# Kernel optimization log

Measured on AMD Instinct MI355X. Metric: run time of the kernel, lower is better.

The kernel has to match this reference:

```python
import jax, jax.numpy as jnp
import numpy as np

V, E, H, L = 32000, 1024, 1024, 2
B, T = 64, 256


def setup_inputs() -> dict:
    key = jax.random.key(0)
    ks = jax.random.split(key, 6)
    src = jax.random.randint(ks[0], (B, T), 0, V, dtype=jnp.int32)
    s_e = 1.0 / np.sqrt(H)
    emb = jax.random.normal(ks[1], (V, E), dtype=jnp.float32) * 0.02
    # stacked-layer LSTM params; layer 0 input = E == H so shapes are uniform
    W_ih = jax.random.uniform(ks[2], (L, 4 * H, H), dtype=jnp.float32, minval=-s_e, maxval=s_e)
    W_hh = jax.random.uniform(ks[3], (L, 4 * H, H), dtype=jnp.float32, minval=-s_e, maxval=s_e)
    b_ih = jax.random.uniform(ks[4], (L, 4 * H), dtype=jnp.float32, minval=-s_e, maxval=s_e)
    b_hh = jax.random.uniform(ks[5], (L, 4 * H), dtype=jnp.float32, minval=-s_e, maxval=s_e)
    return {"src": src, "emb": emb, "W_ih": W_ih, "W_hh": W_hh, "b_ih": b_ih, "b_hh": b_hh}


def _lstm_stack(embedded, W_ih, W_hh, b_ih, b_hh):
    # embedded: [B, T, E]
    Bsz = embedded.shape[0]
    h0 = jnp.zeros((L, Bsz, H), embedded.dtype)
    c0 = jnp.zeros((L, Bsz, H), embedded.dtype)

    def step(carry, x_t):
        h, c = carry  # each [L, B, H]
        x = x_t       # [B, E]
        new_h, new_c = [], []
        for l in range(L):
            gates = x @ W_ih[l].T + b_ih[l] + h[l] @ W_hh[l].T + b_hh[l]  # [B, 4H]
            i, f, g, o = jnp.split(gates, 4, axis=-1)
            c_t = jax.nn.sigmoid(f) * c[l] + jax.nn.sigmoid(i) * jnp.tanh(g)
            h_t = jax.nn.sigmoid(o) * jnp.tanh(c_t)
            new_h.append(h_t)
            new_c.append(c_t)
            x = h_t  # feed to next layer (dropout p=0)
        return (jnp.stack(new_h), jnp.stack(new_c)), x

    (h_n, c_n), outs = jax.lax.scan(step, (h0, c0), jnp.swapaxes(embedded, 0, 1))
    return jnp.swapaxes(outs, 0, 1), h_n, c_n  # [B,T,H], [L,B,H], [L,B,H]


def reference(src, emb, W_ih, W_hh, b_ih, b_hh):
    embedded = emb[src]  # [B, T, E]
    encoder_outputs, h_n, c_n = _lstm_stack(embedded, W_ih, W_hh, b_ih, b_hh)
    return encoder_outputs, (h_n, c_n)
```

## Files before the change

kernel.cpp:

```cpp
#include <hip/hip_runtime.h>
#include <hip/hip_bf16.h>

typedef __hip_bfloat16 bf16;
typedef __attribute__((ext_vector_type(8))) short s16x8;
typedef __attribute__((ext_vector_type(4))) float f32x4;
typedef __attribute__((ext_vector_type(4))) int   i32x4;

#define BATCH   64
#define SEQ     256
#define HID     1024
#define GATES   4096
#define NWG     256
#define THREADS 256
#define UNITS   8
#define NCOLS   32
#define ROWSTRIDE 2056
#define GSTRIDE 33
#define BH      (BATCH * HID)

#define H0_SLOTS 4
#define H1_SLOTS 2
#define FLAG_ELEMS ((size_t)6 * BH)
#define WS_BYTES  (FLAG_ELEMS * 2 + 256 * 4)

#define OUT_HN  ((size_t)BATCH * SEQ * HID)
#define OUT_CN  (OUT_HN + 2ull * BATCH * HID)

__device__ __forceinline__ short f2bf(float f) {
    unsigned int u = __builtin_bit_cast(unsigned int, f);
    u = (u + 0x7fffu + ((u >> 16) & 1u)) >> 16;
    return (short)u;
}

__device__ __forceinline__ void st8(void* p, float lo, float hi) {
    union { float f[2]; unsigned long long u; } v;
    v.f[0] = lo; v.f[1] = hi;
    __hip_atomic_store((unsigned long long*)p, v.u, __ATOMIC_RELAXED, __HIP_MEMORY_SCOPE_AGENT);
}

#define MM8(B0) \
    _Pragma("unroll") \
    for (int kk = (B0); kk < (B0) + 8; ++kk) { \
        s16x8 b0 = *(const s16x8*)(s0 + kk * 32); \
        s16x8 b1 = *(const s16x8*)(s1 + kk * 32); \
        s16x8 av = __builtin_bit_cast(s16x8, h[kk]); \
        a0 = __builtin_amdgcn_mfma_f32_16x16x32_bf16(av, b0, a0, 0, 0, 0); \
        a1 = __builtin_amdgcn_mfma_f32_16x16x32_bf16(av, b1, a1, 0, 0, 0); \
    }

__device__ __forceinline__ void gemm_bt(const bf16* xrow, const bf16* s0, const bf16* s1,
                                        f32x4& a0, f32x4& a1)
{
    i32x4 h[32];
#define LD(i, OFF) asm volatile("global_load_dwordx4 %0, %1, off offset:" OFF " sc0" \
                                : "=v"(h[i]) : "v"(xrow))
    LD(0, "0");    LD(1, "64");   LD(2, "128");  LD(3, "192");
    LD(4, "256");  LD(5, "320");  LD(6, "384");  LD(7, "448");
    LD(8, "512");  LD(9, "576");  LD(10, "640"); LD(11, "704");
    LD(12, "768"); LD(13, "832"); LD(14, "896"); LD(15, "960");
    LD(16, "1024"); LD(17, "1088"); LD(18, "1152"); LD(19, "1216");
    LD(20, "1280"); LD(21, "1344"); LD(22, "1408"); LD(23, "1472");
    asm volatile("s_waitcnt vmcnt(16)"); __builtin_amdgcn_sched_barrier(0);
    MM8(0)
    LD(24, "1536"); LD(25, "1600"); LD(26, "1664"); LD(27, "1728");
    LD(28, "1792"); LD(29, "1856"); LD(30, "1920"); LD(31, "1984");
    asm volatile("s_waitcnt vmcnt(16)"); __builtin_amdgcn_sched_barrier(0);
    MM8(8)
    asm volatile("s_waitcnt vmcnt(8)");  __builtin_amdgcn_sched_barrier(0);
    MM8(16)
    asm volatile("s_waitcnt vmcnt(0)");  __builtin_amdgcn_sched_barrier(0);
    MM8(24)
#undef LD
}

__device__ __forceinline__ void wait_dual(unsigned int* flags, int tid, int tgtA, int tgtB) {
    const int tgt = (tid < 128) ? tgtA : tgtB;
    if (tgt > 0) {
        unsigned int* p = flags + tid;
        while ((int)__hip_atomic_load(p, __ATOMIC_RELAXED, __HIP_MEMORY_SCOPE_AGENT) < tgt)
            __builtin_amdgcn_s_sleep(1);
    }
    __syncthreads();
    asm volatile("" ::: "memory");
}

__global__ void ws_init(unsigned int* p, int n) {
    for (int i = blockIdx.x * blockDim.x + threadIdx.x; i < n; i += gridDim.x * blockDim.x)
        p[i] = 0u;
}

__global__ void __launch_bounds__(THREADS, 1)
lstm_enc(const int* __restrict__ src, const float* __restrict__ Wemb,
         const float* __restrict__ Wih, const float* __restrict__ Whh,
         const float* __restrict__ bih, const float* __restrict__ bhh,
         float* __restrict__ out, bf16* __restrict__ hbuf)
{
    __shared__ __align__(16) bf16 slab[NCOLS][ROWSTRIDE];
    __shared__ float gates[BATCH][GSTRIDE];
    __shared__ float bias[NCOLS];

    const int wg    = blockIdx.x;
    const int layer = wg >> 7;
    const int wgl   = wg & 127;
    const int j0    = wgl * UNITS;
    const int tid   = threadIdx.x;
    const int lane  = tid & 63;
    const int wave  = tid >> 6;
    const int m     = lane & 15;
    const int kq    = (lane >> 4) * 8;
    const int b_a   = wave * 16 + m;

    for (int r = 0; r < NCOLS; ++r) {
        int g = r >> 3, u = r & 7;
        size_t grow = (size_t)layer * GATES * HID + (size_t)(g * HID + j0 + u) * HID;
        int k = tid * 8;
        const float* s = (k < HID) ? (Wih + grow + k) : (Whh + grow + (k - HID));
        s16x8 v;
#pragma unroll
        for (int j = 0; j < 8; ++j) v[j] = f2bf(s[j]);
        *(s16x8*)&slab[r][k] = v;
    }
    if (tid < NCOLS) {
        int g = tid >> 3, u = tid & 7;
        int off = layer * GATES + g * HID + j0 + u;
        bias[tid] = bih[off] + bhh[off];
    }
    __syncthreads();

    __builtin_amdgcn_fence(__ATOMIC_ACQUIRE, "agent");

    bf16* h0 = hbuf;
    bf16* h1 = hbuf + H0_SLOTS * BH;
    unsigned int* flags = (unsigned int*)(hbuf + FLAG_ELEMS);

    const int bb = tid >> 2;
    const int u0 = (tid & 3) * 2;
    float c_lo = 0.f, c_hi = 0.f;

    int sv = (layer == 0) ? src[b_a * SEQ] : 0;

    for (int t = 0; t < SEQ; ++t) {
        f32x4 acc0 = {0.f, 0.f, 0.f, 0.f};
        f32x4 acc1 = {0.f, 0.f, 0.f, 0.f};

        if (layer == 0) {
            const float* xF = Wemb + (size_t)sv * HID + kq;
            if (t + 1 < SEQ) sv = src[b_a * SEQ + t + 1];
#pragma unroll
            for (int c = 0; c < 4; ++c) {
                f32x4 xv[16];
#pragma unroll
                for (int i = 0; i < 8; ++i) {
                    const float* p = xF + (c * 8 + i) * 32;
                    xv[2 * i]     = *(const f32x4*)p;
                    xv[2 * i + 1] = *(const f32x4*)(p + 4);
                }
#pragma unroll
                for (int i = 0; i < 8; ++i) {
                    const int k = (c * 8 + i) * 32 + kq;
                    s16x8 af;
#pragma unroll
                    for (int j = 0; j < 4; ++j) {
                        af[j]     = f2bf(xv[2 * i][j]);
                        af[4 + j] = f2bf(xv[2 * i + 1][j]);
                    }
                    s16x8 b0 = *(const s16x8*)&slab[m][k];
                    s16x8 b1 = *(const s16x8*)&slab[16 + m][k];
                    acc0 = __builtin_amdgcn_mfma_f32_16x16x32_bf16(af, b0, acc0, 0, 0, 0);
                    acc1 = __builtin_amdgcn_mfma_f32_16x16x32_bf16(af, b1, acc1, 0, 0, 0);
                }
            }
            wait_dual(flags, tid, t, t - 3);
        } else {
            wait_dual(flags, tid, t + 1, t);
        }

        if (((t + (wg >> 3)) & 7) == 0)
            __builtin_amdgcn_fence(__ATOMIC_ACQUIRE, "agent");

        if (layer == 0) {
            gemm_bt(h0 + (size_t)((t - 1) & (H0_SLOTS - 1)) * BH + b_a * HID + kq,
                    &slab[m][HID + kq], &slab[16 + m][HID + kq], acc0, acc1);
        } else {
            gemm_bt(h0 + (size_t)(t & (H0_SLOTS - 1)) * BH + b_a * HID + kq,
                    &slab[m][kq], &slab[16 + m][kq], acc0, acc1);
            gemm_bt(h1 + (size_t)((t - 1) & (H1_SLOTS - 1)) * BH + b_a * HID + kq,
                    &slab[m][HID + kq], &slab[16 + m][HID + kq], acc0, acc1);
        }

        const int rowg = wave * 16 + (lane >> 4) * 4;
#pragma unroll
        for (int r = 0; r < 4; ++r) {
            gates[rowg + r][m]      = acc0[r];
            gates[rowg + r][16 + m] = acc1[r];
        }
        __syncthreads();

        {
            float gi0 = gates[bb][u0]      + bias[u0];
            float gi1 = gates[bb][u0 + 1]  + bias[u0 + 1];
            float gf0 = gates[bb][u0 + 8]  + bias[u0 + 8];
            float gf1 = gates[bb][u0 + 9]  + bias[u0 + 9];
            float gg0 = gates[bb][u0 + 16] + bias[u0 + 16];
            float gg1 = gates[bb][u0 + 17] + bias[u0 + 17];
            float go0 = gates[bb][u0 + 24] + bias[u0 + 24];
            float go1 = gates[bb][u0 + 25] + bias[u0 + 25];
            float si0 = 1.f / (1.f + __expf(-gi0)), si1 = 1.f / (1.f + __expf(-gi1));
            float sf0 = 1.f / (1.f + __expf(-gf0)), sf1 = 1.f / (1.f + __expf(-gf1));
            float so0 = 1.f / (1.f + __expf(-go0)), so1 = 1.f / (1.f + __expf(-go1));
            float tg0 = tanhf(gg0), tg1 = tanhf(gg1);
            c_lo = sf0 * c_lo + si0 * tg0;
            c_hi = sf1 * c_hi + si1 * tg1;
            float h_lo = so0 * tanhf(c_lo);
            float h_hi = so1 * tanhf(c_hi);

            bf16* hw = ((layer == 0) ? h0 + (size_t)(t & (H0_SLOTS - 1)) * BH
                                     : h1 + (size_t)(t & (H1_SLOTS - 1)) * BH);
            unsigned int hp = (unsigned int)(unsigned short)f2bf(h_lo) |
                              ((unsigned int)(unsigned short)f2bf(h_hi) << 16);
            __hip_atomic_store((unsigned int*)(hw + bb * HID + j0 + u0), hp,
                               __ATOMIC_RELAXED, __HIP_MEMORY_SCOPE_AGENT);
            if (layer == 1)
                st8(out + ((size_t)bb * SEQ + t) * HID + j0 + u0, h_lo, h_hi);
            if (t == SEQ - 1) {
                size_t o = ((size_t)layer * BATCH + bb) * HID + j0 + u0;
                st8(out + OUT_HN + o, h_lo, h_hi);
                st8(out + OUT_CN + o, c_lo, c_hi);
            }
        }
        __syncthreads();
        asm volatile("" ::: "memory");
        if (tid == 0)
            __hip_atomic_store(flags + wg, (unsigned int)(t + 1),
                               __ATOMIC_RELAXED, __HIP_MEMORY_SCOPE_AGENT);
    }
}

extern "C" void kernel_launch(void* const* d_in, const int* in_sizes, int n_in,
                              void* d_out, int out_size, void* d_ws, size_t ws_size,
                              hipStream_t stream) {
    const int*   src  = (const int*)d_in[0];
    const float* emb  = (const float*)d_in[1];
    const float* W_ih = (const float*)d_in[2];
    const float* W_hh = (const float*)d_in[3];
    const float* b_ih = (const float*)d_in[4];
    const float* b_hh = (const float*)d_in[5];
    float* out  = (float*)d_out;
    bf16*  hbuf = (bf16*)d_ws;

    unsigned int* wsp = (unsigned int*)d_ws;
    int n = (int)(WS_BYTES / 4);
    ws_init<<<256, 256, 0, stream>>>(wsp, n);

    void* args[] = {&src, &emb, &W_ih, &W_hh, &b_ih, &b_hh, &out, &hbuf};
    hipLaunchCooperativeKernel((void*)lstm_enc, dim3(NWG), dim3(THREADS),
                               args, 0, stream);
}
```

Baseline: 3.876 ms.

## Split input and recurrent GEMMs across two wave groups with per-wave flag polling

Doubles the block to 512 threads. One group of four waves computes the input-side projection (embedding or layer-0 h) into its own gate buffer, while the other group computes the recurrent h·W_hh product into a second buffer, so the two halves run concurrently instead of one after the other. The block-wide flag wait is replaced by per-wave polling that checks only the flags each group needs, and the periodic acquire fences are dropped. Global loads of h now carry sc0 sc1 to bypass caches, and the output stores are moved after the flag release. The split adds LDS traffic and block barriers, and the weaker memory ordering may carry a coherence risk.

New measurement: 4.162 ms. 1.07x slower.

```diff
diff --git a/kernel.cpp b/kernel.cpp
--- a/kernel.cpp
+++ b/kernel.cpp
@@ -11,11 +11,11 @@
 #define HID     1024
 #define GATES   4096
 #define NWG     256
-#define THREADS 256
+#define THREADS 512
 #define UNITS   8
 #define NCOLS   32
 #define ROWSTRIDE 2056
-#define GSTRIDE 33
+#define GSTRIDE 36
 #define BH      (BATCH * HID)
 
 #define H0_SLOTS 4
@@ -30,12 +30,6 @@
     unsigned int u = __builtin_bit_cast(unsigned int, f);
     u = (u + 0x7fffu + ((u >> 16) & 1u)) >> 16;
     return (short)u;
-}
-
-__device__ __forceinline__ void st8(void* p, float lo, float hi) {
-    union { float f[2]; unsigned long long u; } v;
-    v.f[0] = lo; v.f[1] = hi;
-    __hip_atomic_store((unsigned long long*)p, v.u, __ATOMIC_RELAXED, __HIP_MEMORY_SCOPE_AGENT);
 }
 
 #define MM8(B0) \
@@ -52,7 +46,7 @@
                                         f32x4& a0, f32x4& a1)
 {
     i32x4 h[32];
-#define LD(i, OFF) asm volatile("global_load_dwordx4 %0, %1, off offset:" OFF " sc0" \
+#define LD(i, OFF) asm volatile("global_load_dwordx4 %0, %1, off offset:" OFF " sc0 sc1" \
                                 : "=v"(h[i]) : "v"(xrow))
     LD(0, "0");    LD(1, "64");   LD(2, "128");  LD(3, "192");
     LD(4, "256");  LD(5, "320");  LD(6, "384");  LD(7, "448");
@@ -73,14 +67,17 @@
 #undef LD
 }
 
-__device__ __forceinline__ void wait_dual(unsigned int* flags, int tid, int tgtA, int tgtB) {
-    const int tgt = (tid < 128) ? tgtA : tgtB;
-    if (tgt > 0) {
-        unsigned int* p = flags + tid;
-        while ((int)__hip_atomic_load(p, __ATOMIC_RELAXED, __HIP_MEMORY_SCOPE_AGENT) < tgt)
-            __builtin_amdgcn_s_sleep(1);
-    }
-    __syncthreads();
+__device__ __forceinline__ void wave_poll(unsigned int* f, int tgt) {
+    if (tgt <= 0) return;
+    const int l = threadIdx.x & 63;
+    unsigned int* p0 = f + l;
+    unsigned int* p1 = f + 64 + l;
+    for (;;) {
+        int a = (int)__hip_atomic_load(p0, __ATOMIC_RELAXED, __HIP_MEMORY_SCOPE_AGENT);
+        int b = (int)__hip_atomic_load(p1, __ATOMIC_RELAXED, __HIP_MEMORY_SCOPE_AGENT);
+        if (__all((a >= tgt) && (b >= tgt))) break;
+        __builtin_amdgcn_s_sleep(1);
+    }
     asm volatile("" ::: "memory");
 }
 
@@ -96,7 +93,8 @@
          float* __restrict__ out, bf16* __restrict__ hbuf)
 {
     __shared__ __align__(16) bf16 slab[NCOLS][ROWSTRIDE];
-    __shared__ float gates[BATCH][GSTRIDE];
+    __shared__ float gx[BATCH][GSTRIDE];
+    __shared__ float gh[BATCH][GSTRIDE];
     __shared__ float bias[NCOLS];
 
     const int wg    = blockIdx.x;
@@ -106,14 +104,16 @@
     const int tid   = threadIdx.x;
     const int lane  = tid & 63;
     const int wave  = tid >> 6;
+    const int grpB  = wave >> 2;
+    const int w4    = wave & 3;
     const int m     = lane & 15;
     const int kq    = (lane >> 4) * 8;
-    const int b_a   = wave * 16 + m;
-
-    for (int r = 0; r < NCOLS; ++r) {
+    const int b_a   = w4 * 16 + m;
+
+    for (int r = (tid >> 8); r < NCOLS; r += 2) {
         int g = r >> 3, u = r & 7;
         size_t grow = (size_t)layer * GATES * HID + (size_t)(g * HID + j0 + u) * HID;
-        int k = tid * 8;
+        int k = (tid & 255) * 8;
         const float* s = (k < HID) ? (Wih + grow + k) : (Whh + grow + (k - HID));
         s16x8 v;
 #pragma unroll
@@ -127,112 +127,106 @@
     }
     __syncthreads();
 
-    __builtin_amdgcn_fence(__ATOMIC_ACQUIRE, "agent");
-
     bf16* h0 = hbuf;
     bf16* h1 = hbuf + H0_SLOTS * BH;
     unsigned int* flags = (unsigned int*)(hbuf + FLAG_ELEMS);
-
-    const int bb = tid >> 2;
-    const int u0 = (tid & 3) * 2;
-    float c_lo = 0.f, c_hi = 0.f;
-
-    int sv = (layer == 0) ? src[b_a * SEQ] : 0;
+    unsigned int* f0 = flags;
+    unsigned int* f1 = flags + 128;
+
+    const int bb = tid >> 3;
+    const int u0 = tid & 7;
+    float c_st = 0.f;
+
+    int sv = (layer == 0 && grpB == 0) ? src[b_a * SEQ] : 0;
 
     for (int t = 0; t < SEQ; ++t) {
         f32x4 acc0 = {0.f, 0.f, 0.f, 0.f};
         f32x4 acc1 = {0.f, 0.f, 0.f, 0.f};
 
-        if (layer == 0) {
-            const float* xF = Wemb + (size_t)sv * HID + kq;
-            if (t + 1 < SEQ) sv = src[b_a * SEQ + t + 1];
-#pragma unroll
-            for (int c = 0; c < 4; ++c) {
-                f32x4 xv[16];
-#pragma unroll
-                for (int i = 0; i < 8; ++i) {
-                    const float* p = xF + (c * 8 + i) * 32;
-                    xv[2 * i]     = *(const f32x4*)p;
-                    xv[2 * i + 1] = *(const f32x4*)(p + 4);
+        if (grpB == 0) {
+            if (layer == 0) {
+                const float* xF = Wemb + (size_t)sv * HID + kq;
+                if (t + 1 < SEQ) sv = src[b_a * SEQ + t + 1];
+#pragma unroll
+                for (int c = 0; c < 4; ++c) {
+                    f32x4 xv[16];
+#pragma unroll
+                    for (int i = 0; i < 8; ++i) {
+                        const float* p = xF + (c * 8 + i) * 32;
+                        xv[2 * i]     = *(const f32x4*)p;
+                        xv[2 * i + 1] = *(const f32x4*)(p + 4);
+                    }
+#pragma unroll
+                    for (int i = 0; i < 8; ++i) {
+                        const int k = (c * 8 + i) * 32 + kq;
+                        s16x8 af;
+#pragma unroll
+                        for (int j = 0; j < 4; ++j) {
+                            af[j]     = f2bf(xv[2 * i][j]);
+                            af[4 + j] = f2bf(xv[2 * i + 1][j]);
+                        }
+                        s16x8 b0 = *(const s16x8*)&slab[m][k];
+                        s16x8 b1 = *(const s16x8*)&slab[16 + m][k];
+                        acc0 = __builtin_amdgcn_mfma_f32_16x16x32_bf16(af, b0, acc0, 0, 0, 0);
+                        acc1 = __builtin_amdgcn_mfma_f32_16x16x32_bf16(af, b1, acc1, 0, 0, 0);
+                    }
                 }
-#pragma unroll
-                for (int i = 0; i < 8; ++i) {
-                    const int k = (c * 8 + i) * 32 + kq;
-                    s16x8 af;
-#pragma unroll
-                    for (int j = 0; j < 4; ++j) {
-                        af[j]     = f2bf(xv[2 * i][j]);
-                        af[4 + j] = f2bf(xv[2 * i + 1][j]);
-                    }
-                    s16x8 b0 = *(const s16x8*)&slab[m][k];
-                    s16x8 b1 = *(const s16x8*)&slab[16 + m][k];
-                    acc0 = __builtin_amdgcn_mfma_f32_16x16x32_bf16(af, b0, acc0, 0, 0, 0);
-                    acc1 = __builtin_amdgcn_mfma_f32_16x16x32_bf16(af, b1, acc1, 0, 0, 0);
-                }
+                wave_poll(f1, t - 3);
+            } else {
+                wave_poll(f0, t + 1);
+                gemm_bt(h0 + (size_t)(t & (H0_SLOTS - 1)) * BH + b_a * HID + kq,
+                        &slab[m][kq], &slab[16 + m][kq], acc0, acc1);
             }
-            wait_dual(flags, tid, t, t - 3);
+            const int rowg = w4 * 16 + (lane >> 4) * 4;
+#pragma unroll
+            for (int r = 0; r < 4; ++r) {
+                gx[rowg + r][m]      = acc0[r];
+                gx[rowg + r][16 + m] = acc1[r];
+            }
         } else {
-            wait_dual(flags, tid, t + 1, t);
-        }
-
-        if (((t + (wg >> 3)) & 7) == 0)
-            __builtin_amdgcn_fence(__ATOMIC_ACQUIRE, "agent");
-
-        if (layer == 0) {
-            gemm_bt(h0 + (size_t)((t - 1) & (H0_SLOTS - 1)) * BH + b_a * HID + kq,
-                    &slab[m][HID + kq], &slab[16 + m][HID + kq], acc0, acc1);
-        } else {
-            gemm_bt(h0 + (size_t)(t & (H0_SLOTS - 1)) * BH + b_a * HID + kq,
-                    &slab[m][kq], &slab[16 + m][kq], acc0, acc1);
-            gemm_bt(h1 + (size_t)((t - 1) & (H1_SLOTS - 1)) * BH + b_a * HID + kq,
-                    &slab[m][HID + kq], &slab[16 + m][HID + kq], acc0, acc1);
-        }
-
-        const int rowg = wave * 16 + (lane >> 4) * 4;
-#pragma unroll
-        for (int r = 0; r < 4; ++r) {
-            gates[rowg + r][m]      = acc0[r];
-            gates[rowg + r][16 + m] = acc1[r];
+            wave_poll(layer == 0 ? f0 : f1, t);
+            bf16* hrow = ((layer == 0)
+                ? h0 + (size_t)((t - 1) & (H0_SLOTS - 1)) * BH
+                : h1 + (size_t)((t - 1) & (H1_SLOTS - 1)) * BH) + b_a * HID + kq;
+            gemm_bt(hrow, &slab[m][HID + kq], &slab[16 + m][HID + kq], acc0, acc1);
+            const int rowg = w4 * 16 + (lane >> 4) * 4;
+#pragma unroll
+            for (int r = 0; r < 4; ++r) {
+                gh[rowg + r][m]      = acc0[r];
+                gh[rowg + r][16 + m] = acc1[r];
+            }
         }
         __syncthreads();
 
-        {
-            float gi0 = gates[bb][u0]      + bias[u0];
-            float gi1 = gates[bb][u0 + 1]  + bias[u0 + 1];
-            float gf0 = gates[bb][u0 + 8]  + bias[u0 + 8];
-            float gf1 = gates[bb][u0 + 9]  + bias[u0 + 9];
-            float gg0 = gates[bb][u0 + 16] + bias[u0 + 16];
-            float gg1 = gates[bb][u0 + 17] + bias[u0 + 17];
-            float go0 = gates[bb][u0 + 24] + bias[u0 + 24];
-            float go1 = gates[bb][u0 + 25] + bias[u0 + 25];
-            float si0 = 1.f / (1.f + __expf(-gi0)), si1 = 1.f / (1.f + __expf(-gi1));
-            float sf0 = 1.f / (1.f + __expf(-gf0)), sf1 = 1.f / (1.f + __expf(-gf1));
-            float so0 = 1.f / (1.f + __expf(-go0)), so1 = 1.f / (1.f + __expf(-go1));
-            float tg0 = tanhf(gg0), tg1 = tanhf(gg1);
-            c_lo = sf0 * c_lo + si0 * tg0;
-            c_hi = sf1 * c_hi + si1 * tg1;
-            float h_lo = so0 * tanhf(c_lo);
-            float h_hi = so1 * tanhf(c_hi);
-
-            bf16* hw = ((layer == 0) ? h0 + (size_t)(t & (H0_SLOTS - 1)) * BH
-                                     : h1 + (size_t)(t & (H1_SLOTS - 1)) * BH);
-            unsigned int hp = (unsigned int)(unsigned short)f2bf(h_lo) |
-                              ((unsigned int)(unsigned short)f2bf(h_hi) << 16);
-            __hip_atomic_store((unsigned int*)(hw + bb * HID + j0 + u0), hp,
-                               __ATOMIC_RELAXED, __HIP_MEMORY_SCOPE_AGENT);
-            if (layer == 1)
-                st8(out + ((size_t)bb * SEQ + t) * HID + j0 + u0, h_lo, h_hi);
-            if (t == SEQ - 1) {
-                size_t o = ((size_t)layer * BATCH + bb) * HID + j0 + u0;
-                st8(out + OUT_HN + o, h_lo, h_hi);
-                st8(out + OUT_CN + o, c_lo, c_hi);
-            }
-        }
+        float gi = gx[bb][u0]      + gh[bb][u0]      + bias[u0];
+        float gf = gx[bb][u0 + 8]  + gh[bb][u0 + 8]  + bias[u0 + 8];
+        float gg = gx[bb][u0 + 16] + gh[bb][u0 + 16] + bias[u0 + 16];
+        float go = gx[bb][u0 + 24] + gh[bb][u0 + 24] + bias[u0 + 24];
+        float si = 1.f / (1.f + __expf(-gi));
+        float sf = 1.f / (1.f + __expf(-gf));
+        float so = 1.f / (1.f + __expf(-go));
+        c_st = sf * c_st + si * tanhf(gg);
+        float h_v = so * tanhf(c_st);
+
+        bf16* hw = ((layer == 0) ? h0 + (size_t)(t & (H0_SLOTS - 1)) * BH
+                                 : h1 + (size_t)(t & (H1_SLOTS - 1)) * BH);
+        __hip_atomic_store((unsigned short*)(hw + bb * HID + j0 + u0),
+                           (unsigned short)f2bf(h_v),
+                           __ATOMIC_RELAXED, __HIP_MEMORY_SCOPE_AGENT);
+
         __syncthreads();
         asm volatile("" ::: "memory");
         if (tid == 0)
             __hip_atomic_store(flags + wg, (unsigned int)(t + 1),
                                __ATOMIC_RELAXED, __HIP_MEMORY_SCOPE_AGENT);
+
+        if (layer == 1)
+            out[((size_t)bb * SEQ + t) * HID + j0 + u0] = h_v;
+        if (t == SEQ - 1) {
+            size_t o = ((size_t)layer * BATCH + bb) * HID + j0 + u0;
+            out[OUT_HN + o] = h_v;
+            out[OUT_CN + o] = c_st;
+        }
     }
 }
 
```

## Route layer-0 hidden state through output buffer and use per-wave flag polling

Applied to the files above, without the earlier changes.

Layer 0 now writes its fp32 hidden state into out[b, t+4] rows, which layer 1 later overwrites, instead of into a bf16 ring buffer. Both layers read it back with fp32 loads converted to bf16. The block-wide wait plus syncthreads is replaced by per-wave polling with __all, and layer 1 waits on the layer-0 flags and the layer-1 flags separately. This lets the input GEMM overlap with waiting on the recurrent flags. The h loads gain sc1, the periodic acquire fences are removed, and the output and final-state stores become plain stores issued after the flag release. This aims to cut synchronisation latency on the critical path. It relies on relaxed ordering and cache-bypass loads for correctness, and the slot-reuse timing in the output buffer is delicate.

After: 4.535 ms. +17.0%, slower.

```diff
diff --git a/kernel.cpp b/kernel.cpp
--- a/kernel.cpp
+++ b/kernel.cpp
@@ -38,6 +38,35 @@
     __hip_atomic_store((unsigned long long*)p, v.u, __ATOMIC_RELAXED, __HIP_MEMORY_SCOPE_AGENT);
 }
 
+__device__ __forceinline__ void gemm_f32c(const float* xrow, const bf16* s0, const bf16* s1,
+                                          f32x4& a0, f32x4& a1)
+{
+#pragma unroll
+    for (int c = 0; c < 4; ++c) {
+        f32x4 xv[16];
+#pragma unroll
+        for (int i = 0; i < 8; ++i) {
+            const float* p = xrow + (c * 8 + i) * 32;
+            xv[2 * i]     = *(const f32x4*)p;
+            xv[2 * i + 1] = *(const f32x4*)(p + 4);
+        }
+#pragma unroll
+        for (int i = 0; i < 8; ++i) {
+            const int kk = c * 8 + i;
+            s16x8 af;
+#pragma unroll
+            for (int j = 0; j < 4; ++j) {
+                af[j]     = f2bf(xv[2 * i][j]);
+                af[4 + j] = f2bf(xv[2 * i + 1][j]);
+            }
+            s16x8 b0 = *(const s16x8*)(s0 + kk * 32);
+            s16x8 b1 = *(const s16x8*)(s1 + kk * 32);
+            a0 = __builtin_amdgcn_mfma_f32_16x16x32_bf16(af, b0, a0, 0, 0, 0);
+            a1 = __builtin_amdgcn_mfma_f32_16x16x32_bf16(af, b1, a1, 0, 0, 0);
+        }
+    }
+}
+
 #define MM8(B0) \
     _Pragma("unroll") \
     for (int kk = (B0); kk < (B0) + 8; ++kk) { \
@@ -52,7 +81,7 @@
                                         f32x4& a0, f32x4& a1)
 {
     i32x4 h[32];
-#define LD(i, OFF) asm volatile("global_load_dwordx4 %0, %1, off offset:" OFF " sc0" \
+#define LD(i, OFF) asm volatile("global_load_dwordx4 %0, %1, off offset:" OFF " sc0 sc1" \
                                 : "=v"(h[i]) : "v"(xrow))
     LD(0, "0");    LD(1, "64");   LD(2, "128");  LD(3, "192");
     LD(4, "256");  LD(5, "320");  LD(6, "384");  LD(7, "448");
@@ -73,14 +102,17 @@
 #undef LD
 }
 
-__device__ __forceinline__ void wait_dual(unsigned int* flags, int tid, int tgtA, int tgtB) {
-    const int tgt = (tid < 128) ? tgtA : tgtB;
-    if (tgt > 0) {
-        unsigned int* p = flags + tid;
-        while ((int)__hip_atomic_load(p, __ATOMIC_RELAXED, __HIP_MEMORY_SCOPE_AGENT) < tgt)
-            __builtin_amdgcn_s_sleep(1);
-    }
-    __syncthreads();
+__device__ __forceinline__ void wave_poll(unsigned int* f, int tgt) {
+    if (tgt <= 0) return;
+    const int l = threadIdx.x & 63;
+    unsigned int* p0 = f + l;
+    unsigned int* p1 = f + 64 + l;
+    for (;;) {
+        int a = (int)__hip_atomic_load(p0, __ATOMIC_RELAXED, __HIP_MEMORY_SCOPE_AGENT);
+        int b = (int)__hip_atomic_load(p1, __ATOMIC_RELAXED, __HIP_MEMORY_SCOPE_AGENT);
+        if (__all((a >= tgt) && (b >= tgt))) break;
+        __builtin_amdgcn_s_sleep(1);
+    }
     asm volatile("" ::: "memory");
 }
 
@@ -127,11 +159,11 @@
     }
     __syncthreads();
 
-    __builtin_amdgcn_fence(__ATOMIC_ACQUIRE, "agent");
-
     bf16* h0 = hbuf;
     bf16* h1 = hbuf + H0_SLOTS * BH;
     unsigned int* flags = (unsigned int*)(hbuf + FLAG_ELEMS);
+    unsigned int* f0 = flags;
+    unsigned int* f1 = flags + 128;
 
     const int bb = tid >> 2;
     const int u0 = (tid & 3) * 2;
@@ -146,46 +178,28 @@
         if (layer == 0) {
             const float* xF = Wemb + (size_t)sv * HID + kq;
             if (t + 1 < SEQ) sv = src[b_a * SEQ + t + 1];
-#pragma unroll
-            for (int c = 0; c < 4; ++c) {
-                f32x4 xv[16];
-#pragma unroll
-                for (int i = 0; i < 8; ++i) {
-                    const float* p = xF + (c * 8 + i) * 32;
-                    xv[2 * i]     = *(const f32x4*)p;
-                    xv[2 * i + 1] = *(const f32x4*)(p + 4);
-                }
-#pragma unroll
-                for (int i = 0; i < 8; ++i) {
-                    const int k = (c * 8 + i) * 32 + kq;
-                    s16x8 af;
-#pragma unroll
-                    for (int j = 0; j < 4; ++j) {
-                        af[j]     = f2bf(xv[2 * i][j]);
-                        af[4 + j] = f2bf(xv[2 * i + 1][j]);
-                    }
-                    s16x8 b0 = *(const s16x8*)&slab[m][k];
-                    s16x8 b1 = *(const s16x8*)&slab[16 + m][k];
-                    acc0 = __builtin_amdgcn_mfma_f32_16x16x32_bf16(af, b0, acc0, 0, 0, 0);
-                    acc1 = __builtin_amdgcn_mfma_f32_16x16x32_bf16(af, b1, acc1, 0, 0, 0);
-                }
+            gemm_f32c(xF, &slab[m][kq], &slab[16 + m][kq], acc0, acc1);
+            wave_poll(f0, t);
+            if (t >= 1) {
+                if (t <= 252)
+                    gemm_f32c(out + ((size_t)b_a * SEQ + (t + 3)) * HID + kq,
+                              &slab[m][HID + kq], &slab[16 + m][HID + kq], acc0, acc1);
+                else
+                    gemm_bt(h0 + (size_t)((t - 1) & 3) * BH + b_a * HID + kq,
+                            &slab[m][HID + kq], &slab[16 + m][HID + kq], acc0, acc1);
             }
-            wait_dual(flags, tid, t, t - 3);
         } else {
-            wait_dual(flags, tid, t + 1, t);
-        }
-
-        if (((t + (wg >> 3)) & 7) == 0)
-            __builtin_amdgcn_fence(__ATOMIC_ACQUIRE, "agent");
-
-        if (layer == 0) {
-            gemm_bt(h0 + (size_t)((t - 1) & (H0_SLOTS - 1)) * BH + b_a * HID + kq,
-                    &slab[m][HID + kq], &slab[16 + m][HID + kq], acc0, acc1);
-        } else {
-            gemm_bt(h0 + (size_t)(t & (H0_SLOTS - 1)) * BH + b_a * HID + kq,
-                    &slab[m][kq], &slab[16 + m][kq], acc0, acc1);
-            gemm_bt(h1 + (size_t)((t - 1) & (H1_SLOTS - 1)) * BH + b_a * HID + kq,
-                    &slab[m][HID + kq], &slab[16 + m][HID + kq], acc0, acc1);
+            wave_poll(f0, t + 1);
+            if (t <= 251)
+                gemm_f32c(out + ((size_t)b_a * SEQ + (t + 4)) * HID + kq,
+                          &slab[m][kq], &slab[16 + m][kq], acc0, acc1);
+            else
+                gemm_bt(h0 + (size_t)(t & 3) * BH + b_a * HID + kq,
+                        &slab[m][kq], &slab[16 + m][kq], acc0, acc1);
+            wave_poll(f1, t);
+            if (t >= 1)
+                gemm_bt(h1 + (size_t)((t - 1) & 1) * BH + b_a * HID + kq,
+                        &slab[m][HID + kq], &slab[16 + m][HID + kq], acc0, acc1);
         }
 
         const int rowg = wave * 16 + (lane >> 4) * 4;
@@ -196,43 +210,52 @@
         }
         __syncthreads();
 
-        {
-            float gi0 = gates[bb][u0]      + bias[u0];
-            float gi1 = gates[bb][u0 + 1]  + bias[u0 + 1];
-            float gf0 = gates[bb][u0 + 8]  + bias[u0 + 8];
-            float gf1 = gates[bb][u0 + 9]  + bias[u0 + 9];
-            float gg0 = gates[bb][u0 + 16] + bias[u0 + 16];
-            float gg1 = gates[bb][u0 + 17] + bias[u0 + 17];
-            float go0 = gates[bb][u0 + 24] + bias[u0 + 24];
-            float go1 = gates[bb][u0 + 25] + bias[u0 + 25];
-            float si0 = 1.f / (1.f + __expf(-gi0)), si1 = 1.f / (1.f + __expf(-gi1));
-            float sf0 = 1.f / (1.f + __expf(-gf0)), sf1 = 1.f / (1.f + __expf(-gf1));
-            float so0 = 1.f / (1.f + __expf(-go0)), so1 = 1.f / (1.f + __expf(-go1));
-            float tg0 = tanhf(gg0), tg1 = tanhf(gg1);
-            c_lo = sf0 * c_lo + si0 * tg0;
-            c_hi = sf1 * c_hi + si1 * tg1;
-            float h_lo = so0 * tanhf(c_lo);
-            float h_hi = so1 * tanhf(c_hi);
-
-            bf16* hw = ((layer == 0) ? h0 + (size_t)(t & (H0_SLOTS - 1)) * BH
-                                     : h1 + (size_t)(t & (H1_SLOTS - 1)) * BH);
+        float gi0 = gates[bb][u0]      + bias[u0];
+        float gi1 = gates[bb][u0 + 1]  + bias[u0 + 1];
+        float gf0 = gates[bb][u0 + 8]  + bias[u0 + 8];
+        float gf1 = gates[bb][u0 + 9]  + bias[u0 + 9];
+        float gg0 = gates[bb][u0 + 16] + bias[u0 + 16];
+        float gg1 = gates[bb][u0 + 17] + bias[u0 + 17];
+        float go0 = gates[bb][u0 + 24] + bias[u0 + 24];
+        float go1 = gates[bb][u0 + 25] + bias[u0 + 25];
+        float si0 = 1.f / (1.f + __expf(-gi0)), si1 = 1.f / (1.f + __expf(-gi1));
+        float sf0 = 1.f / (1.f + __expf(-gf0)), sf1 = 1.f / (1.f + __expf(-gf1));
+        float so0 = 1.f / (1.f + __expf(-go0)), so1 = 1.f / (1.f + __expf(-go1));
+        float tg0 = tanhf(gg0), tg1 = tanhf(gg1);
+        c_lo = sf0 * c_lo + si0 * tg0;
+        c_hi = sf1 * c_hi + si1 * tg1;
+        float h_lo = so0 * tanhf(c_lo);
+        float h_hi = so1 * tanhf(c_hi);
+
+        if (layer == 0) {
+            if (t <= 251)
+                st8(out + ((size_t)bb * SEQ + (t + 4)) * HID + j0 + u0, h_lo, h_hi);
+            else {
+                unsigned int hp = (unsigned int)(unsigned short)f2bf(h_lo) |
+                                  ((unsigned int)(unsigned short)f2bf(h_hi) << 16);
+                __hip_atomic_store((unsigned int*)(h0 + (size_t)(t & 3) * BH + bb * HID + j0 + u0),
+                                   hp, __ATOMIC_RELAXED, __HIP_MEMORY_SCOPE_AGENT);
+            }
+        } else {
             unsigned int hp = (unsigned int)(unsigned short)f2bf(h_lo) |
                               ((unsigned int)(unsigned short)f2bf(h_hi) << 16);
-            __hip_atomic_store((unsigned int*)(hw + bb * HID + j0 + u0), hp,
-                               __ATOMIC_RELAXED, __HIP_MEMORY_SCOPE_AGENT);
-            if (layer == 1)
-                st8(out + ((size_t)bb * SEQ + t) * HID + j0 + u0, h_lo, h_hi);
-            if (t == SEQ - 1) {
-                size_t o = ((size_t)layer * BATCH + bb) * HID + j0 + u0;
-                st8(out + OUT_HN + o, h_lo, h_hi);
-                st8(out + OUT_CN + o, c_lo, c_hi);
-            }
-        }
+            __hip_atomic_store((unsigned int*)(h1 + (size_t)(t & 1) * BH + bb * HID + j0 + u0),
+                               hp, __ATOMIC_RELAXED, __HIP_MEMORY_SCOPE_AGENT);
+        }
+
         __syncthreads();
         asm volatile("" ::: "memory");
         if (tid == 0)
             __hip_atomic_store(flags + wg, (unsigned int)(t + 1),
                                __ATOMIC_RELAXED, __HIP_MEMORY_SCOPE_AGENT);
+
+        if (layer == 1)
+            *(float2*)(out + ((size_t)bb * SEQ + t) * HID + j0 + u0) = make_float2(h_lo, h_hi);
+        if (t == SEQ - 1) {
+            size_t o = ((size_t)layer * BATCH + bb) * HID + j0 + u0;
+            *(float2*)(out + OUT_HN + o) = make_float2(h_lo, h_hi);
+            *(float2*)(out + OUT_CN + o) = make_float2(c_lo, c_hi);
+        }
     }
 }
 
```
